# Optimization experiments

Measured on AMD Instinct MI355X. Metric: run time of the kernel, lower is better.

## Reference

```python
import jax, jax.numpy as jnp
import numpy as np
from jax import lax

# Static problem sizes (see shape_source): 128 events x 512 points each
G, P, K = 128, 512, 16          # graphs, points per graph, knn k
FEAT = 128                       # n_samples*2
PLANES = [128, 96, 64, 32]       # linear reduction, n_graph=3, graph_out=32
N_OUT = 3                        # n_type


def setup_inputs() -> dict:
    key = jax.random.key(0)
    ks = jax.random.split(key, 24)
    N = G * P
    x = jax.random.normal(ks[0], (N, FEAT), jnp.float32)
    # coo: integer detector coords (cols 0,1) + graph id (col 2)
    xy = jax.random.randint(ks[1], (N, 2), 0, 32).astype(jnp.int32)
    gid = jnp.repeat(jnp.arange(G, dtype=jnp.int32), P)
    coo = jnp.concatenate([xy, gid[:, None]], axis=1)  # [N,3]
    inp = {"x": x, "coo": coo}
    # SAGEConv params per layer: lin_l (neighbor-mean path, with bias), lin_r (root path)
    ki = 2
    for l, (nin, nout) in enumerate(zip(PLANES[:-1], PLANES[1:])):
        s = 1.0 / np.sqrt(nin)
        inp[f"wl{l}"] = jax.random.normal(ks[ki], (nin, nout), jnp.float32) * s; ki += 1
        inp[f"wr{l}"] = jax.random.normal(ks[ki], (nin, nout), jnp.float32) * s; ki += 1
        inp[f"b{l}"] = jnp.zeros((nout,), jnp.float32)
    # MLP head: 32 -> 32 -> 3 with ReLU between (n_lin = 2)
    inp["lw0"] = jax.random.normal(ks[ki], (PLANES[-1], PLANES[-1]), jnp.float32) / np.sqrt(PLANES[-1]); ki += 1
    inp["lb0"] = jnp.zeros((PLANES[-1],), jnp.float32)
    inp["lw1"] = jax.random.normal(ks[ki], (PLANES[-1], N_OUT), jnp.float32) / np.sqrt(PLANES[-1]); ki += 1
    inp["lb1"] = jnp.zeros((N_OUT,), jnp.float32)
    return inp


def _knn_indices(coo):
    # knn_graph(coo, k, batch=coo[:,2], loop=False): k nearest within each graph,
    # self excluded. Batch segments are uniform size P so reshape per-graph.
    pos = coo.reshape(G, P, 3).astype(jnp.float32)
    d2 = jnp.sum((pos[:, :, None, :] - pos[:, None, :, :]) ** 2, axis=-1)  # [G,P,P]
    d2 = jnp.where(jnp.eye(P, dtype=bool), jnp.inf, d2)  # loop=False
    _, idx = lax.top_k(-d2, K)  # [G,P,K] neighbor (source) indices per target
    return idx


def reference(x, coo, wl0, wr0, b0, wl1, wr1, b1, wl2, wr2, b2, lw0, lb0, lw1, lb1):
    idx = _knn_indices(coo)
    h = x.reshape(G, P, FEAT)
    gather = jax.vmap(lambda hg, ig: hg[ig])  # per-graph neighbor gather
    for wl, wr, b in ((wl0, wr0, b0), (wl1, wr1, b1), (wl2, wr2, b2)):
        nbr_mean = gather(h, idx).mean(axis=2)  # [G,P,K,nin] -> [G,P,nin]
        # SAGEConv: lin_l(mean_j x_j) + lin_r(x_i), then ReLU (GraphLayer)
        h = jax.nn.relu(jnp.einsum('gpi,io->gpo', nbr_mean, wl)
                        + jnp.einsum('gpi,io->gpo', h, wr) + b)
    pooled = h.max(axis=1)  # global_max_pool over batch -> [G, 32]
    hid = jax.nn.relu(pooled @ lw0 + lb0)
    return hid @ lw1 + lb1  # [G, 3]
```

## Files before the change

kernel.cpp:

```cpp
#include <hip/hip_runtime.h>

#define G 128
#define P 512
#define K 16
#define NPTS (G * P)

typedef _Float16 half8 __attribute__((ext_vector_type(8)));
typedef float    floatx4 __attribute__((ext_vector_type(4)));

__device__ __forceinline__ unsigned uminu(unsigned a, unsigned b) { return a < b ? a : b; }

__device__ __forceinline__ void ce(unsigned& a, unsigned& b) {
    const unsigned lo = a < b ? a : b;
    const unsigned hi = a < b ? b : a;
    a = lo; b = hi;
}

__device__ __forceinline__ void sort16(unsigned k[16]) {
#pragma unroll
    for (int p = 1; p < 16; p <<= 1) {
#pragma unroll
        for (int q = p; q >= 1; q >>= 1) {
#pragma unroll
            for (int j = q % p; j + q < 16; j += 2 * q) {
#pragma unroll
                for (int i = 0; i < q; ++i) {
                    const int a = i + j, b2 = i + j + q;
                    if (b2 < 16 && (a / (2 * p)) == (b2 / (2 * p)))
                        ce(k[a], k[b2]);
                }
            }
        }
    }
}

__device__ __forceinline__ void halfmerge(unsigned best[16], const unsigned kb[16]) {
#pragma unroll
    for (int i = 0; i < 16; ++i) best[i] = uminu(best[i], kb[15 - i]);
#pragma unroll
    for (int d = 8; d >= 1; d >>= 1)
#pragma unroll
        for (int i = 0; i < 16; ++i)
            if ((i & d) == 0) ce(best[i], best[i + d]);
}

__global__ __launch_bounds__(512, 8)
void knn_kernel(const int* __restrict__ coo, int* __restrict__ idx_out) {
    __shared__ float2 sxy[P];
    __shared__ unsigned mk[4][64][17];
    const int b   = blockIdx.x;
    const int g   = b >> 3;
    const int t0  = (b & 7) * 64;
    const int tid = threadIdx.x;
    const int tgt = tid & 63;
    const int sub = tid >> 6;

    for (int i = tid; i < P; i += 512) {
        const int* cp = coo + (size_t)(g * P + i) * 3;
        sxy[i] = make_float2((float)cp[0], (float)cp[1]);
    }
    __syncthreads();

    const int tg = t0 + tgt;
    const float px = sxy[tg].x, py = sxy[tg].y;

    unsigned best[K];
#pragma unroll
    for (int k = 0; k < K; ++k) best[k] = 0xFFFFFFF0u + k;

    const int s0 = sub * 64;
#pragma unroll 1
    for (int batch = 0; batch < 4; ++batch) {
        unsigned kb[K];
#pragma unroll
        for (int j = 0; j < 16; ++j) {
            const int s = s0 + batch * 16 + j;
            const float2 c = sxy[s];
            const float dx = px - c.x, dy = py - c.y;
            const float keyf = fmaf(fmaf(dx, dx, dy * dy), 512.f, (float)s);
            unsigned key = (unsigned)keyf;
            if (s == tg) key = 0xFFFFFFFFu;
            kb[j] = key;
        }
        sort16(kb);
        halfmerge(best, kb);
    }

    if (sub >= 4) {
#pragma unroll
        for (int k = 0; k < K; ++k) mk[sub - 4][tgt][k] = best[k];
    }
    __syncthreads();
    if (sub < 4) {
        unsigned pb[K];
#pragma unroll
        for (int k = 0; k < K; ++k) pb[k] = mk[sub][tgt][k];
        halfmerge(best, pb);
    }
    __syncthreads();
    if (sub == 2 || sub == 3) {
#pragma unroll
        for (int k = 0; k < K; ++k) mk[sub - 2][tgt][k] = best[k];
    }
    __syncthreads();
    if (sub < 2) {
        unsigned pb[K];
#pragma unroll
        for (int k = 0; k < K; ++k) pb[k] = mk[sub][tgt][k];
        halfmerge(best, pb);
    }
    __syncthreads();
    if (sub == 1) {
#pragma unroll
        for (int k = 0; k < K; ++k) mk[0][tgt][k] = best[k];
    }
    __syncthreads();
    if (sub == 0) {
        unsigned pb[K];
#pragma unroll
        for (int k = 0; k < K; ++k) pb[k] = mk[0][tgt][k];
        halfmerge(best, pb);
        int4* op = (int4*)(idx_out + (size_t)(g * P + tg) * K);
#pragma unroll
        for (int q4 = 0; q4 < 4; ++q4) {
            int4 o;
            o.x = (int)(best[q4 * 4 + 0] & (unsigned)(P - 1));
            o.y = (int)(best[q4 * 4 + 1] & (unsigned)(P - 1));
            o.z = (int)(best[q4 * 4 + 2] & (unsigned)(P - 1));
            o.w = (int)(best[q4 * 4 + 3] & (unsigned)(P - 1));
            op[q4] = o;
        }
    }
}

__global__ __launch_bounds__(256)
void cvt_kernel(const float* __restrict__ x, _Float16* __restrict__ x16, int n8) {
    const int i = blockIdx.x * 256 + threadIdx.x;
    if (i >= n8) return;
    const float4* p = (const float4*)(x + (size_t)i * 8);
    const float4 a = p[0], bq = p[1];
    half8 o;
    o[0] = (_Float16)a.x;  o[1] = (_Float16)a.y;
    o[2] = (_Float16)a.z;  o[3] = (_Float16)a.w;
    o[4] = (_Float16)bq.x; o[5] = (_Float16)bq.y;
    o[6] = (_Float16)bq.z; o[7] = (_Float16)bq.w;
    *(half8*)(x16 + (size_t)i * 8) = o;
}

template <int KT, int NIN, int NOUT>
__device__ __forceinline__ void prep_body(int b, int tid,
                                          const float* __restrict__ wl,
                                          const float* __restrict__ wr,
                                          _Float16* __restrict__ wf) {
    const int e = b * 256 + tid;
    const int fr   = e >> 9;
    const int lane = (e >> 3) & 63;
    const int j    = e & 7;
    const int ntile = fr / KT;
    const int kt    = fr - ntile * KT;
    const int k = kt * 32 + ((lane >> 4) << 3) + j;
    const int n = ntile * 16 + (lane & 15);
    const float v = (k < NIN) ? wl[k * NOUT + n] : wr[(k - NIN) * NOUT + n];
    wf[e] = (_Float16)v;
}

__global__ __launch_bounds__(256)
void prep_all_kernel(const float* __restrict__ wl0, const float* __restrict__ wr0,
                     const float* __restrict__ wl1, const float* __restrict__ wr1,
                     const float* __restrict__ wl2, const float* __restrict__ wr2,
                     _Float16* __restrict__ wf0, _Float16* __restrict__ wf1,
                     _Float16* __restrict__ wf2) {
    const int b = blockIdx.x;
    const int t = threadIdx.x;
    if (b < 96)       prep_body<8, 128, 96>(b,       t, wl0, wr0, wf0);
    else if (b < 144) prep_body<6,  96, 64>(b - 96,  t, wl1, wr1, wf1);
    else              prep_body<4,  64, 32>(b - 144, t, wl2, wr2, wf2);
}

template <int CIN, int NOUT, bool FOUT16>
__global__ __launch_bounds__(256, 4)
void sage_kernel(const _Float16* __restrict__ hin, const int* __restrict__ idxg,
                 const _Float16* __restrict__ wf, const float* __restrict__ bias,
                 void* __restrict__ hout) {
    constexpr int KTm = CIN / 32;
    constexpr int KT  = CIN / 16;
    constexpr int NH  = NOUT / 32;
    constexpr int RS  = 136;

    __shared__ _Float16 As[64 * RS];

    const int tid  = threadIdx.x;
    const int b    = blockIdx.x;
    const int slot = b >> 3;
    const int g    = (b & 7) | ((slot & 15) << 3);
    const int n0   = g * P + (slot >> 4) * 64;
    const _Float16* __restrict__ hg = hin + (size_t)(g * P) * CIN;

    const int pt = tid >> 2;
    const int q  = tid & 3;

    const int4* ip = (const int4*)(idxg + (size_t)(n0 + pt) * K);
    const int4 na = ip[0], nb4 = ip[1], nc = ip[2], nd = ip[3];
    const int nn[16] = {na.x, na.y, na.z, na.w, nb4.x, nb4.y, nb4.z, nb4.w,
                        nc.x, nc.y, nc.z, nc.w, nd.x, nd.y, nd.z, nd.w};

#pragma unroll 1
    for (int c = 0; c < KTm; ++c) {
        const int ch = c * 32 + q * 8;
        half8 a0 = {}; half8 a1 = {};
#pragma unroll
        for (int k = 0; k < 16; k += 4) {
            const half8 v0 = *(const half8*)(hg + (size_t)nn[k + 0] * CIN + ch);
            const half8 v1 = *(const half8*)(hg + (size_t)nn[k + 1] * CIN + ch);
            const half8 v2 = *(const half8*)(hg + (size_t)nn[k + 2] * CIN + ch);
            const half8 v3 = *(const half8*)(hg + (size_t)nn[k + 3] * CIN + ch);
            a0 += v0; a1 += v1; a0 += v2; a1 += v3;
        }
        half8 m;
#pragma unroll
        for (int e = 0; e < 8; ++e)
            m[e] = (_Float16)(((float)a0[e] + (float)a1[e]) * 0.0625f);
        *(half8*)&As[pt * RS + (c * 4 + q) * 8] = m;
    }

    const int l  = tid & 63;
    const int wv = tid >> 6;
    const int mh = wv & 1;
    const int nh = wv >> 1;
    const int lm = l & 15, lq = l >> 4;

    float bs[NH];
#pragma unroll
    for (int nt = 0; nt < NH; ++nt)
        bs[nt] = bias[nh * (NOUT / 2) + nt * 16 + lm];

    __syncthreads();

    floatx4 acc[2][NH];
#pragma unroll
    for (int mt = 0; mt < 2; ++mt)
#pragma unroll
        for (int nt = 0; nt < NH; ++nt) {
            floatx4 z = {0.f, 0.f, 0.f, 0.f};
            acc[mt][nt] = z;
        }

#pragma unroll
    for (int kt = 0; kt < KT; ++kt) {
        half8 bfr[NH];
#pragma unroll
        for (int nt = 0; nt < NH; ++nt) {
            const int ng = nh * NH + nt;
            bfr[nt] = *(const half8*)(wf + ((size_t)(ng * KT + kt) * 64 + l) * 8);
        }
#pragma unroll
        for (int mt = 0; mt < 2; ++mt) {
            const int row = mh * 32 + mt * 16 + lm;
            half8 a;
            if (kt < KTm) {
                a = *(const half8*)&As[row * RS + (kt * 4 + lq) * 8];
            } else {
                a = *(const half8*)(hin + (size_t)(n0 + row) * CIN +
                                    (kt - KTm) * 32 + lq * 8);
            }
#pragma unroll
            for (int nt = 0; nt < NH; ++nt)
                acc[mt][nt] = __builtin_amdgcn_mfma_f32_16x16x32_f16(
                    a, bfr[nt], acc[mt][nt], 0, 0, 0);
        }
    }

#pragma unroll
    for (int mt = 0; mt < 2; ++mt)
#pragma unroll
        for (int nt = 0; nt < NH; ++nt) {
            const int n = nh * (NOUT / 2) + nt * 16 + lm;
#pragma unroll
            for (int r = 0; r < 4; ++r) {
                const int p = n0 + mh * 32 + mt * 16 + lq * 4 + r;
                float v = acc[mt][nt][r] + bs[nt];
                v = v > 0.f ? v : 0.f;
                if constexpr (FOUT16)
                    ((_Float16*)hout)[(size_t)p * NOUT + n] = (_Float16)v;
                else
                    ((float*)hout)[(size_t)p * NOUT + n] = v;
            }
        }
}

__global__ __launch_bounds__(256)
void head_kernel(const _Float16* __restrict__ h3, const float* __restrict__ lw0,
                 const float* __restrict__ lb0, const float* __restrict__ lw1,
                 const float* __restrict__ lb1, float* __restrict__ out) {
    __shared__ float red[256];
    __shared__ float pooled[32];
    __shared__ float hid[32];
    const int g = blockIdx.x;
    const int t = threadIdx.x;
    const int c = t & 31;
    const int r = t >> 5;

    const _Float16* hb = h3 + (size_t)g * P * 32;
    float m = -3.4e38f;
    for (int p = r; p < P; p += 8) m = fmaxf(m, (float)hb[p * 32 + c]);
    red[t] = m;
    __syncthreads();
    if (r < 4) red[t] = fmaxf(red[t], red[t + 128]);
    __syncthreads();
    if (r < 2) red[t] = fmaxf(red[t], red[t + 64]);
    __syncthreads();
    if (r == 0) pooled[c] = fmaxf(red[t], red[t + 32]);
    __syncthreads();

    if (t < 32) {
        float a = lb0[t];
#pragma unroll
        for (int i = 0; i < 32; ++i) a += pooled[i] * lw0[i * 32 + t];
        hid[t] = a > 0.f ? a : 0.f;
    }
    __syncthreads();
    if (t < 3) {
        float a = lb1[t];
#pragma unroll
        for (int i = 0; i < 32; ++i) a += hid[i] * lw1[i * 3 + t];
        out[g * 3 + t] = a;
    }
}

extern "C" void kernel_launch(void* const* d_in, const int* in_sizes, int n_in,
                              void* d_out, int out_size, void* d_ws, size_t ws_size,
                              hipStream_t stream) {
    const float* x   = (const float*)d_in[0];
    const int*   coo = (const int*)  d_in[1];
    const float* wl0 = (const float*)d_in[2];
    const float* wr0 = (const float*)d_in[3];
    const float* b0  = (const float*)d_in[4];
    const float* wl1 = (const float*)d_in[5];
    const float* wr1 = (const float*)d_in[6];
    const float* b1  = (const float*)d_in[7];
    const float* wl2 = (const float*)d_in[8];
    const float* wr2 = (const float*)d_in[9];
    const float* b2  = (const float*)d_in[10];
    const float* lw0 = (const float*)d_in[11];
    const float* lb0 = (const float*)d_in[12];
    const float* lw1 = (const float*)d_in[13];
    const float* lb1 = (const float*)d_in[14];
    float* out = (float*)d_out;

    char* ws = (char*)d_ws;
    _Float16* wf0 = (_Float16*)(ws + 0);
    _Float16* wf1 = (_Float16*)(ws + 49152);
    _Float16* wf2 = (_Float16*)(ws + 73728);
    int*      idx = (int*)     (ws + 81920);
    _Float16* x16 = (_Float16*)(ws + 4276224);
    _Float16* h1  = (_Float16*)(ws + 21053440);
    _Float16* h2  = (_Float16*)(ws + 33636352);
    _Float16* h3  = (_Float16*)(ws + 42024960);

    prep_all_kernel<<<160, 256, 0, stream>>>(wl0, wr0, wl1, wr1, wl2, wr2,
                                             wf0, wf1, wf2);
    cvt_kernel<<<4096, 256, 0, stream>>>(x, x16, NPTS * 128 / 8);
    knn_kernel<<<G * 8, 512, 0, stream>>>(coo, idx);

    sage_kernel<128, 96, true><<<NPTS / 64, 256, 0, stream>>>(x16, idx, wf0, b0, h1);
    sage_kernel< 96, 64, true><<<NPTS / 64, 256, 0, stream>>>(h1,  idx, wf1, b1, h2);
    sage_kernel< 64, 32, true><<<NPTS / 64, 256, 0, stream>>>(h2,  idx, wf2, b2, h3);

    head_kernel<<<G, 256, 0, stream>>>(h3, lw0, lb0, lw1, lb1, out);
}
```

Before: 183.5 us.

## Merge knn, fp16 conversion and weight prep into one pre-kernel launch

Fuses the three independent preprocessing kernels (knn, fp32→fp16 conversion of x, weight repacking) into a single launch with block-index dispatch, so the pieces run concurrently and two launches disappear. The knn partial-result merge changes from a three-level tree reduction with several barriers to one barrier and a serial seven-way merge in the first sub-group. The batch loop is also fully unrolled. The serial merge lengthens the critical path for one wave, larger shared memory (7 slots) and the 4-block launch bound may cut knn occupancy, and full unrolling raises register pressure.

```diff
diff --git a/kernel.cpp b/kernel.cpp
--- a/kernel.cpp
+++ b/kernel.cpp
@@ -44,115 +44,10 @@
             if ((i & d) == 0) ce(best[i], best[i + d]);
 }
 
-__global__ __launch_bounds__(512, 8)
-void knn_kernel(const int* __restrict__ coo, int* __restrict__ idx_out) {
-    __shared__ float2 sxy[P];
-    __shared__ unsigned mk[4][64][17];
-    const int b   = blockIdx.x;
-    const int g   = b >> 3;
-    const int t0  = (b & 7) * 64;
-    const int tid = threadIdx.x;
-    const int tgt = tid & 63;
-    const int sub = tid >> 6;
-
-    for (int i = tid; i < P; i += 512) {
-        const int* cp = coo + (size_t)(g * P + i) * 3;
-        sxy[i] = make_float2((float)cp[0], (float)cp[1]);
-    }
-    __syncthreads();
-
-    const int tg = t0 + tgt;
-    const float px = sxy[tg].x, py = sxy[tg].y;
-
-    unsigned best[K];
-#pragma unroll
-    for (int k = 0; k < K; ++k) best[k] = 0xFFFFFFF0u + k;
-
-    const int s0 = sub * 64;
-#pragma unroll 1
-    for (int batch = 0; batch < 4; ++batch) {
-        unsigned kb[K];
-#pragma unroll
-        for (int j = 0; j < 16; ++j) {
-            const int s = s0 + batch * 16 + j;
-            const float2 c = sxy[s];
-            const float dx = px - c.x, dy = py - c.y;
-            const float keyf = fmaf(fmaf(dx, dx, dy * dy), 512.f, (float)s);
-            unsigned key = (unsigned)keyf;
-            if (s == tg) key = 0xFFFFFFFFu;
-            kb[j] = key;
-        }
-        sort16(kb);
-        halfmerge(best, kb);
-    }
-
-    if (sub >= 4) {
-#pragma unroll
-        for (int k = 0; k < K; ++k) mk[sub - 4][tgt][k] = best[k];
-    }
-    __syncthreads();
-    if (sub < 4) {
-        unsigned pb[K];
-#pragma unroll
-        for (int k = 0; k < K; ++k) pb[k] = mk[sub][tgt][k];
-        halfmerge(best, pb);
-    }
-    __syncthreads();
-    if (sub == 2 || sub == 3) {
-#pragma unroll
-        for (int k = 0; k < K; ++k) mk[sub - 2][tgt][k] = best[k];
-    }
-    __syncthreads();
-    if (sub < 2) {
-        unsigned pb[K];
-#pragma unroll
-        for (int k = 0; k < K; ++k) pb[k] = mk[sub][tgt][k];
-        halfmerge(best, pb);
-    }
-    __syncthreads();
-    if (sub == 1) {
-#pragma unroll
-        for (int k = 0; k < K; ++k) mk[0][tgt][k] = best[k];
-    }
-    __syncthreads();
-    if (sub == 0) {
-        unsigned pb[K];
-#pragma unroll
-        for (int k = 0; k < K; ++k) pb[k] = mk[0][tgt][k];
-        halfmerge(best, pb);
-        int4* op = (int4*)(idx_out + (size_t)(g * P + tg) * K);
-#pragma unroll
-        for (int q4 = 0; q4 < 4; ++q4) {
-            int4 o;
-            o.x = (int)(best[q4 * 4 + 0] & (unsigned)(P - 1));
-            o.y = (int)(best[q4 * 4 + 1] & (unsigned)(P - 1));
-            o.z = (int)(best[q4 * 4 + 2] & (unsigned)(P - 1));
-            o.w = (int)(best[q4 * 4 + 3] & (unsigned)(P - 1));
-            op[q4] = o;
-        }
-    }
-}
-
-__global__ __launch_bounds__(256)
-void cvt_kernel(const float* __restrict__ x, _Float16* __restrict__ x16, int n8) {
-    const int i = blockIdx.x * 256 + threadIdx.x;
-    if (i >= n8) return;
-    const float4* p = (const float4*)(x + (size_t)i * 8);
-    const float4 a = p[0], bq = p[1];
-    half8 o;
-    o[0] = (_Float16)a.x;  o[1] = (_Float16)a.y;
-    o[2] = (_Float16)a.z;  o[3] = (_Float16)a.w;
-    o[4] = (_Float16)bq.x; o[5] = (_Float16)bq.y;
-    o[6] = (_Float16)bq.z; o[7] = (_Float16)bq.w;
-    *(half8*)(x16 + (size_t)i * 8) = o;
-}
-
 template <int KT, int NIN, int NOUT>
-__device__ __forceinline__ void prep_body(int b, int tid,
-                                          const float* __restrict__ wl,
+__device__ __forceinline__ void prep_elem(int e, const float* __restrict__ wl,
                                           const float* __restrict__ wr,
                                           _Float16* __restrict__ wf) {
-    const int e = b * 256 + tid;
     const int fr   = e >> 9;
     const int lane = (e >> 3) & 63;
     const int j    = e & 7;
@@ -164,17 +59,96 @@
     wf[e] = (_Float16)v;
 }
 
-__global__ __launch_bounds__(256)
-void prep_all_kernel(const float* __restrict__ wl0, const float* __restrict__ wr0,
-                     const float* __restrict__ wl1, const float* __restrict__ wr1,
-                     const float* __restrict__ wl2, const float* __restrict__ wr2,
-                     _Float16* __restrict__ wf0, _Float16* __restrict__ wf1,
-                     _Float16* __restrict__ wf2) {
-    const int b = blockIdx.x;
-    const int t = threadIdx.x;
-    if (b < 96)       prep_body<8, 128, 96>(b,       t, wl0, wr0, wf0);
-    else if (b < 144) prep_body<6,  96, 64>(b - 96,  t, wl1, wr1, wf1);
-    else              prep_body<4,  64, 32>(b - 144, t, wl2, wr2, wf2);
+__global__ __launch_bounds__(512, 4)
+void pre_kernel(const int* __restrict__ coo, int* __restrict__ idx_out,
+                const float* __restrict__ x, _Float16* __restrict__ x16,
+                const float* __restrict__ wl0, const float* __restrict__ wr0,
+                const float* __restrict__ wl1, const float* __restrict__ wr1,
+                const float* __restrict__ wl2, const float* __restrict__ wr2,
+                _Float16* __restrict__ wf0, _Float16* __restrict__ wf1,
+                _Float16* __restrict__ wf2) {
+    __shared__ float2 sxy[P];
+    __shared__ unsigned mk[7][64][17];
+    const int b   = blockIdx.x;
+    const int tid = threadIdx.x;
+
+    if (b < 1024) {
+        const int g   = b >> 3;
+        const int t0  = (b & 7) * 64;
+        const int tgt = tid & 63;
+        const int sub = tid >> 6;
+
+        for (int i = tid; i < P; i += 512) {
+            const int* cp = coo + (size_t)(g * P + i) * 3;
+            sxy[i] = make_float2((float)cp[0], (float)cp[1]);
+        }
+        __syncthreads();
+
+        const int tg = t0 + tgt;
+        const float px = sxy[tg].x, py = sxy[tg].y;
+
+        unsigned best[K];
+#pragma unroll
+        for (int k = 0; k < K; ++k) best[k] = 0xFFFFFFF0u + k;
+
+        const int s0 = sub * 64;
+#pragma unroll
+        for (int batch = 0; batch < 4; ++batch) {
+            unsigned kb[K];
+#pragma unroll
+            for (int j = 0; j < 16; ++j) {
+                const int s = s0 + batch * 16 + j;
+                const float2 c = sxy[s];
+                const float dx = px - c.x, dy = py - c.y;
+                const float keyf = fmaf(fmaf(dx, dx, dy * dy), 512.f, (float)s);
+                unsigned key = (unsigned)keyf;
+                if (s == tg) key = 0xFFFFFFFFu;
+                kb[j] = key;
+            }
+            sort16(kb);
+            halfmerge(best, kb);
+        }
+
+        if (sub != 0) {
+#pragma unroll
+            for (int k = 0; k < K; ++k) mk[sub - 1][tgt][k] = best[k];
+        }
+        __syncthreads();
+        if (sub == 0) {
+#pragma unroll 1
+            for (int ss = 0; ss < 7; ++ss) {
+                unsigned pb[K];
+#pragma unroll
+                for (int k = 0; k < K; ++k) pb[k] = mk[ss][tgt][k];
+                halfmerge(best, pb);
+            }
+            int4* op = (int4*)(idx_out + (size_t)(g * P + tg) * K);
+#pragma unroll
+            for (int q4 = 0; q4 < 4; ++q4) {
+                int4 o;
+                o.x = (int)(best[q4 * 4 + 0] & (unsigned)(P - 1));
+                o.y = (int)(best[q4 * 4 + 1] & (unsigned)(P - 1));
+                o.z = (int)(best[q4 * 4 + 2] & (unsigned)(P - 1));
+                o.w = (int)(best[q4 * 4 + 3] & (unsigned)(P - 1));
+                op[q4] = o;
+            }
+        }
+    } else if (b < 3072) {
+        const int i = (b - 1024) * 512 + tid;
+        const float4* p = (const float4*)(x + (size_t)i * 8);
+        const float4 a = p[0], bq = p[1];
+        half8 o;
+        o[0] = (_Float16)a.x;  o[1] = (_Float16)a.y;
+        o[2] = (_Float16)a.z;  o[3] = (_Float16)a.w;
+        o[4] = (_Float16)bq.x; o[5] = (_Float16)bq.y;
+        o[6] = (_Float16)bq.z; o[7] = (_Float16)bq.w;
+        *(half8*)(x16 + (size_t)i * 8) = o;
+    } else {
+        const int e = (b - 3072) * 512 + tid;
+        if (e < 24576)      prep_elem<8, 128, 96>(e,         wl0, wr0, wf0);
+        else if (e < 36864) prep_elem<6,  96, 64>(e - 24576, wl1, wr1, wf1);
+        else                prep_elem<4,  64, 32>(e - 36864, wl2, wr2, wf2);
+    }
 }
 
 template <int CIN, int NOUT, bool FOUT16>
@@ -357,10 +331,9 @@
     _Float16* h2  = (_Float16*)(ws + 33636352);
     _Float16* h3  = (_Float16*)(ws + 42024960);
 
-    prep_all_kernel<<<160, 256, 0, stream>>>(wl0, wr0, wl1, wr1, wl2, wr2,
-                                             wf0, wf1, wf2);
-    cvt_kernel<<<4096, 256, 0, stream>>>(x, x16, NPTS * 128 / 8);
-    knn_kernel<<<G * 8, 512, 0, stream>>>(coo, idx);
+    pre_kernel<<<3152, 512, 0, stream>>>(coo, idx, x, x16,
+                                         wl0, wr0, wl1, wr1, wl2, wr2,
+                                         wf0, wf1, wf2);
 
     sage_kernel<128, 96, true><<<NPTS / 64, 256, 0, stream>>>(x16, idx, wf0, b0, h1);
     sage_kernel< 96, 64, true><<<NPTS / 64, 256, 0, stream>>>(h1,  idx, wf1, b1, h2);
```

Result: faster. 172.6 us (-5.9%).
